# Kernel optimization log

Measured on AMD Instinct MI355X. Metric: run time of the kernel, lower is better.

Reference implementation:

```python
import jax, jax.numpy as jnp
import numpy as np
import math

B, S, H = 2, 2048, 2048
NQ, NKV, HD = 16, 4, 128
THETA = 10000.0


def rotate_half(x):
    x1, x2 = jnp.split(x, 2, axis=-1)
    return jnp.concatenate([-x2, x1], axis=-1)


def rope_cos_sin(position_ids, dim, base, dtype):
    # inv_freq: (dim/2,)
    inv_freq = 1.0 / (base ** (jnp.arange(0, dim, 2, dtype=jnp.float32) / dim))
    freqs = position_ids.astype(jnp.float32)[..., None] * inv_freq  # (B, S, dim/2)
    emb = jnp.concatenate([freqs, freqs], axis=-1)  # (B, S, dim)
    return jnp.cos(emb).astype(dtype), jnp.sin(emb).astype(dtype)


def setup_inputs() -> dict:
    key = jax.random.key(0)
    ks = jax.random.split(key, 5)
    hidden_states = jax.random.normal(ks[0], (B, S, H), dtype=jnp.float32)
    position_ids = jnp.broadcast_to(jnp.arange(S, dtype=jnp.int32)[None, :], (B, S))
    sc = 0.02
    wq = jax.random.normal(ks[1], (NQ * HD, H), dtype=jnp.float32) * sc
    wk = jax.random.normal(ks[2], (NKV * HD, H), dtype=jnp.float32) * sc
    wv = jax.random.normal(ks[3], (NKV * HD, H), dtype=jnp.float32) * sc
    wo = jax.random.normal(ks[4], (H, NQ * HD), dtype=jnp.float32) * sc
    return {"hidden_states": hidden_states, "position_ids": position_ids,
            "wq": wq, "wk": wk, "wv": wv, "wo": wo}


def reference(hidden_states, position_ids, wq, wk, wv, wo):
    b, s, _ = hidden_states.shape
    n_rep = NQ // NKV
    # QKV projections (no bias)
    q = (hidden_states @ wq.T).reshape(b, s, NQ, HD).transpose(0, 2, 1, 3)   # (b, nq, s, hd)
    k = (hidden_states @ wk.T).reshape(b, s, NKV, HD).transpose(0, 2, 1, 3)  # (b, nkv, s, hd)
    v = (hidden_states @ wv.T).reshape(b, s, NKV, HD).transpose(0, 2, 1, 3)
    # RoPE (full rotary, partial_rotary_factor == 1.0)
    cos, sin = rope_cos_sin(position_ids, HD, THETA, q.dtype)  # (b, s, hd)
    cos = cos[:, None, :, :]
    sin = sin[:, None, :, :]
    q = q * cos + rotate_half(q) * sin
    k = k * cos + rotate_half(k) * sin
    # repeat_kv for GQA: (b, nkv, s, hd) -> (b, nq, s, hd)
    k = jnp.repeat(k, n_rep, axis=1)
    v = jnp.repeat(v, n_rep, axis=1)
    # scores (b, nq, s, s)
    scores = jnp.einsum('bhqd,bhkd->bhqk', q, k) / math.sqrt(HD)
    causal = jnp.triu(jnp.full((s, s), -jnp.inf, dtype=scores.dtype), k=1)
    scores = scores + causal
    probs = jax.nn.softmax(scores.astype(jnp.float32), axis=-1).astype(q.dtype)
    out = jnp.einsum('bhqk,bhkd->bhqd', probs, v)  # (b, nq, s, hd)
    out = out.transpose(0, 2, 1, 3).reshape(b, s, NQ * HD)
    return out @ wo.T
```

## Files before the change

kernel.cpp:

```cpp
#include <hip/hip_runtime.h>
#include <hip/hip_bf16.h>
#include <cstdint>

typedef unsigned short u16;
typedef __attribute__((ext_vector_type(4))) float f32x4;
typedef __attribute__((ext_vector_type(8))) short s16x8;
typedef __attribute__((ext_vector_type(4))) unsigned int u32x4;
typedef __attribute__((ext_vector_type(2))) unsigned int u32x2;
typedef __attribute__((ext_vector_type(4))) unsigned short u16x4;
typedef __attribute__((ext_vector_type(8))) unsigned short u16x8;

#define MFMA16(a, b, c) __builtin_amdgcn_mfma_f32_16x16x32_bf16(a, b, c, 0, 0, 0)
#define GLOAD16(g, l) __builtin_amdgcn_global_load_lds((const __attribute__((address_space(1))) void*)(g), (__attribute__((address_space(3))) void*)(l), 16, 0, 0)

__device__ __forceinline__ u16 f2bf(float f) {
    union { float f; uint32_t u; } v{f};
    uint32_t r = v.u + 0x7FFF + ((v.u >> 16) & 1);
    return (u16)(r >> 16);
}
__device__ __forceinline__ float bf2f(u16 b) {
    union { uint32_t u; float f; } v;
    v.u = ((uint32_t)b) << 16;
    return v.f;
}

__global__ void cast_f32_bf16(const float* __restrict__ in, u16* __restrict__ out, int n4) {
    int i = blockIdx.x * 256 + threadIdx.x;
    if (i >= n4) return;
    float4 f = ((const float4*)in)[i];
    u16x4 o = { f2bf(f.x), f2bf(f.y), f2bf(f.z), f2bf(f.w) };
    ((u16x4*)out)[i] = o;
}

__global__ void rope_table_k(const int* __restrict__ pos, float* __restrict__ ct, float* __restrict__ st) {
    int i = blockIdx.x * 256 + threadIdx.x;
    int j = i & 63;
    int bs = i >> 6;
    float p = (float)pos[bs];
    float invf = powf(10000.0f, -(float)j * (1.0f / 64.0f));
    float ang = p * invf;
    ct[i] = cosf(ang);
    st[i] = sinf(ang);
}

template <int FUSE>
__global__ __launch_bounds__(256) void gemm_bt(const u16* __restrict__ A, const u16* __restrict__ Bw,
                                               float* __restrict__ C, int M, int N, int K,
                                               const float* __restrict__ ct, const float* __restrict__ st,
                                               u16* __restrict__ Qb, u16* __restrict__ Kb,
                                               u16* __restrict__ Vb) {
    __shared__ u16 Sh[128 * 128];
    u16* As = Sh;
    u16* Bs = Sh + 8192;
    const int tid = threadIdx.x;
    const int lane = tid & 63, wid = tid >> 6;
    const int g = lane >> 4, r = lane & 15;

    const int gx = gridDim.x, nwg = gx * gridDim.y;
    int lid = blockIdx.y * gx + blockIdx.x;
    int swz = (lid % 8) * (nwg / 8) + lid / 8;
    const int bxi = swz % gx, byi = swz / gx;

    const size_t bm = (size_t)byi * 128, bn = (size_t)bxi * 128;
    const int wr = (wid >> 1) * 64, wc = (wid & 1) * 64;

    const int srow = wid * 32 + (lane >> 3);
    const int schunk = (lane & 7) ^ ((lane >> 3) & 7);
    const u16* aSrc = A + (bm + srow) * (size_t)K + schunk * 8;
    const u16* bSrc = Bw + (bn + srow) * (size_t)K + schunk * 8;
    u16* aDst = As + wid * 2048;
    u16* bDst = Bs + wid * 2048;

    f32x4 acc[4][4] = {};
    for (int kt = 0; kt < K; kt += 64) {
#pragma unroll
        for (int j = 0; j < 4; ++j) {
            GLOAD16(aSrc + (size_t)(j * 8) * K + kt, aDst + j * 512);
            GLOAD16(bSrc + (size_t)(j * 8) * K + kt, bDst + j * 512);
        }
        __syncthreads();
        s16x8 af[4][2], bfr[4][2];
#pragma unroll
        for (int m = 0; m < 4; ++m)
#pragma unroll
            for (int kk = 0; kk < 2; ++kk) {
                int rowa = wr + m * 16 + r;
                af[m][kk] = *(const s16x8*)(As + rowa * 64 + (((kk * 4 + g) ^ (rowa & 7)) << 3));
                int rowb = wc + m * 16 + r;
                bfr[m][kk] = *(const s16x8*)(Bs + rowb * 64 + (((kk * 4 + g) ^ (rowb & 7)) << 3));
            }
#pragma unroll
        for (int m = 0; m < 4; ++m)
#pragma unroll
            for (int n = 0; n < 4; ++n) {
                acc[m][n] = MFMA16(af[m][0], bfr[n][0], acc[m][n]);
                acc[m][n] = MFMA16(af[m][1], bfr[n][1], acc[m][n]);
            }
        __syncthreads();
    }
    if (FUSE == 0) {
#pragma unroll
        for (int m = 0; m < 4; ++m)
#pragma unroll
            for (int n = 0; n < 4; ++n)
#pragma unroll
                for (int i = 0; i < 4; ++i) {
                    size_t row = bm + wr + m * 16 + g * 4 + i;
                    size_t col = bn + wc + n * 16 + r;
                    C[row * N + col] = acc[m][n][i];
                }
        return;
    }
#pragma unroll
    for (int m = 0; m < 4; ++m)
#pragma unroll
        for (int n = 0; n < 4; ++n)
#pragma unroll
            for (int i = 0; i < 4; ++i) {
                int rowl = wr + m * 16 + g * 4 + i;
                int col = wc + n * 16 + r;
                int c4 = col >> 3;
                *(u16*)((char*)Sh + rowl * 256 + (((c4 ^ (rowl & 15))) << 4) + ((col & 7) << 1)) =
                    f2bf(acc[m][n][i]);
            }
    __syncthreads();
    if (tid < 128) {
        const int hb = bxi;
        if (hb < 20) {
            const int rowl = tid;
            const size_t tok = bm + rowl;
            const int b = (int)(tok >> 11), s = (int)(tok & 2047);
            u16* dst;
            if (hb < 16) dst = Qb + (((size_t)(b * 16 + hb) * 2048 + s) << 7);
            else         dst = Kb + (((size_t)(b * 4 + (hb - 16)) * 2048 + s) << 7);
            const char* tb = (const char*)Sh + rowl * 256;
            const float* ctr = ct + tok * 64;
            const float* str = st + tok * 64;
#pragma unroll
            for (int c4 = 0; c4 < 8; ++c4) {
                u32x4 lo4 = *(const u32x4*)(tb + ((c4 ^ (rowl & 15)) << 4));
                u32x4 hi4 = *(const u32x4*)(tb + (((c4 + 8) ^ (rowl & 15)) << 4));
                const u16* lo = (const u16*)&lo4;
                const u16* hi = (const u16*)&hi4;
                u16x4 o0, o1, o2, o3;
                u16* olo[2] = { (u16*)&o0, (u16*)&o1 };
                u16* ohi[2] = { (u16*)&o2, (u16*)&o3 };
#pragma unroll
                for (int j = 0; j < 8; ++j) {
                    float c = ctr[c4 * 8 + j], sn = str[c4 * 8 + j];
                    float xl = bf2f(lo[j]), xh = bf2f(hi[j]);
                    olo[j >> 2][j & 3] = f2bf(xl * c - xh * sn);
                    ohi[j >> 2][j & 3] = f2bf(xh * c + xl * sn);
                }
                *(u16x4*)(dst + c4 * 8) = o0;
                *(u16x4*)(dst + c4 * 8 + 4) = o1;
                *(u16x4*)(dst + 64 + c4 * 8) = o2;
                *(u16x4*)(dst + 64 + c4 * 8 + 4) = o3;
            }
        } else {
            const int d = tid;
            const size_t tok0 = bm;
            const int b = (int)(tok0 >> 11), s0 = (int)(tok0 & 2047);
            u16* dst = Vb + (size_t)(b * 4 + (hb - 20)) * 262144 + (size_t)d * 2048 + s0;
            const int dslot = d >> 3, dbyte = (d & 7) << 1;
#pragma unroll
            for (int jb = 0; jb < 16; ++jb) {
                u16x8 v;
#pragma unroll
                for (int jj = 0; jj < 8; ++jj) {
                    int s = jb * 8 + jj;
                    v[jj] = *(const u16*)((const char*)Sh + s * 256 +
                                          (((dslot ^ (s & 15))) << 4) + dbyte);
                }
                *(u16x8*)(dst + jb * 8) = v;
            }
        }
    }
}

__global__ __launch_bounds__(256, 2) void attn_k(const u16* __restrict__ Qb, const u16* __restrict__ Kb,
                                                 const u16* __restrict__ Vb, u16* __restrict__ Ob) {
    __shared__ char smem[49152];
    u16* Ksh = (u16*)smem;
    u16* Vts = (u16*)(smem + 16384);
    char* Pall = smem + 32768;
    const int tid = threadIdx.x;
    const int lane = tid & 63, w = tid >> 6;
    const int g = lane >> 4, r = lane & 15;

    const int lid = blockIdx.y * gridDim.x + blockIdx.x;
    const int cpy = lid >> 8, p = lid & 255;
    const int bh = p & 31;
    const int qblk = cpy ? (7 - (p >> 5)) : ((p >> 5) + 8);

    const int b = bh >> 4, h = bh & 15;
    const int hkv = h >> 2;
    const int q0 = qblk * 128;
    const u16* Qh = Qb + ((size_t)(b * 16 + h) << 18);
    const u16* Kh = Kb + ((size_t)(b * 4 + hkv) << 18);
    const u16* Vh = Vb + ((size_t)(b * 4 + hkv) << 18);

    s16x8 qf[2][4];
#pragma unroll
    for (int qq = 0; qq < 2; ++qq)
#pragma unroll
        for (int c = 0; c < 4; ++c)
            qf[qq][c] = *(const s16x8*)(Qh + (size_t)(q0 + qq * 64 + w * 16 + r) * 128 + c * 32 + g * 8);

    f32x4 o[2][8] = {};
    float mrun[2] = {-1e30f, -1e30f};
    float lrun[2] = {0.f, 0.f};
    const int fmax[2] = { q0 + w * 16 + 15, q0 + 64 + w * 16 + 15 };

    const int ntiles = 2 * qblk + 2;
    const int krow0 = tid >> 4, kch = tid & 15;

    u32x4 kpr[4], vpr[4];
#pragma unroll
    for (int it = 0; it < 4; ++it)
        kpr[it] = *(const u32x4*)(Kh + (size_t)(krow0 + it * 16) * 128 + kch * 8);
#pragma unroll
    for (int it = 0; it < 4; ++it) {
        int task = tid + it * 256;
        vpr[it] = *(const u32x4*)(Vh + (size_t)(task >> 3) * 2048 + (task & 7) * 8);
    }

    for (int t = 0; t < ntiles; ++t) {
        const int kv0 = t * 64;
        __syncthreads();
#pragma unroll
        for (int it = 0; it < 4; ++it) {
            int row = krow0 + it * 16;
            *(u32x4*)((char*)Ksh + row * 256 + ((kch ^ (row & 7)) << 4)) = kpr[it];
        }
#pragma unroll
        for (int it = 0; it < 4; ++it) {
            int task = tid + it * 256;
            int d = task >> 3, ch = task & 7;
            *(u32x4*)((char*)Vts + d * 128 + ((ch ^ (d & 7) ^ ((d >> 3) & 7)) << 4)) = vpr[it];
        }
        __syncthreads();
        if (t + 1 < ntiles) {
            const int kn = kv0 + 64;
#pragma unroll
            for (int it = 0; it < 4; ++it)
                kpr[it] = *(const u32x4*)(Kh + (size_t)(kn + krow0 + it * 16) * 128 + kch * 8);
#pragma unroll
            for (int it = 0; it < 4; ++it) {
                int task = tid + it * 256;
                vpr[it] = *(const u32x4*)(Vh + (size_t)(task >> 3) * 2048 + kn + (task & 7) * 8);
            }
        }
        f32x4 st4[2][4];
#pragma unroll
        for (int ts = 0; ts < 4; ++ts) {
            int row = ts * 16 + r;
            s16x8 kf[4];
#pragma unroll
            for (int c = 0; c < 4; ++c)
                kf[c] = *(const s16x8*)((const char*)Ksh + row * 256 + (((c * 4 + g) ^ (row & 7)) << 4));
            f32x4 a0 = {}, a1 = {};
            if (kv0 <= fmax[0])
#pragma unroll
                for (int c = 0; c < 4; ++c) a0 = MFMA16(kf[c], qf[0][c], a0);
            if (kv0 <= fmax[1])
#pragma unroll
                for (int c = 0; c < 4; ++c) a1 = MFMA16(kf[c], qf[1][c], a1);
            st4[0][ts] = a0;
            st4[1][ts] = a1;
        }
#pragma unroll
        for (int qq = 0; qq < 2; ++qq) {
            if (kv0 > fmax[qq]) continue;
            const int qg = q0 + qq * 64 + w * 16 + r;
            float sv[16];
            float mtile = -1e30f;
#pragma unroll
            for (int ts = 0; ts < 4; ++ts)
#pragma unroll
                for (int i = 0; i < 4; ++i) {
                    int kvg = kv0 + ts * 16 + g * 4 + i;
                    float s = st4[qq][ts][i] * 0.08838834764831845f;
                    s = (kvg > qg) ? -1e30f : s;
                    sv[ts * 4 + i] = s;
                    mtile = fmaxf(mtile, s);
                }
            mtile = fmaxf(mtile, __shfl_xor(mtile, 16));
            mtile = fmaxf(mtile, __shfl_xor(mtile, 32));
            float mnew = fmaxf(mrun[qq], mtile);
            float corr = __expf(mrun[qq] - mnew);
            float psum = 0.f;
            unsigned int pw[8];
#pragma unroll
            for (int ts = 0; ts < 4; ++ts) {
                float p0 = __expf(sv[ts * 4 + 0] - mnew);
                float p1 = __expf(sv[ts * 4 + 1] - mnew);
                float p2 = __expf(sv[ts * 4 + 2] - mnew);
                float p3 = __expf(sv[ts * 4 + 3] - mnew);
                psum += (p0 + p1) + (p2 + p3);
                pw[ts * 2 + 0] = (unsigned int)f2bf(p0) | ((unsigned int)f2bf(p1) << 16);
                pw[ts * 2 + 1] = (unsigned int)f2bf(p2) | ((unsigned int)f2bf(p3) << 16);
            }
            psum += __shfl_xor(psum, 16);
            psum += __shfl_xor(psum, 32);
            lrun[qq] = lrun[qq] * corr + psum;
            mrun[qq] = mnew;
#pragma unroll
            for (int dsb = 0; dsb < 8; ++dsb)
#pragma unroll
                for (int i = 0; i < 4; ++i) o[qq][dsb][i] *= corr;
            char* pbase = Pall + (w * 2 + qq) * 2048;
#pragma unroll
            for (int ts = 0; ts < 4; ++ts) {
                int chunk = (ts * 2 + (g >> 1)) ^ (r & 7);
                u32x2 val = { pw[ts * 2], pw[ts * 2 + 1] };
                *(u32x2*)(pbase + r * 128 + chunk * 16 + (g & 1) * 8) = val;
            }
        }
        asm volatile("s_waitcnt lgkmcnt(0)" ::: "memory");
#pragma unroll
        for (int c = 0; c < 2; ++c) {
            s16x8 vf[8];
#pragma unroll
            for (int dsb = 0; dsb < 8; ++dsb) {
                int d = dsb * 16 + r;
                vf[dsb] = *(const s16x8*)((const char*)Vts + d * 128 +
                    ((((c * 4 + g) ^ (d & 7) ^ ((d >> 3) & 7))) << 4));
            }
#pragma unroll
            for (int qq = 0; qq < 2; ++qq) {
                if (kv0 > fmax[qq]) continue;
                s16x8 pf = *(const s16x8*)(Pall + (w * 2 + qq) * 2048 + r * 128 +
                                           (((c * 4 + g) ^ (r & 7)) << 4));
#pragma unroll
                for (int dsb = 0; dsb < 8; ++dsb)
                    o[qq][dsb] = MFMA16(vf[dsb], pf, o[qq][dsb]);
            }
        }
    }
    __syncthreads();
#pragma unroll
    for (int qq = 0; qq < 2; ++qq) {
        float linv = 1.0f / lrun[qq];
        char* obase = smem + (w << 13) + (qq << 12);
#pragma unroll
        for (int dsb = 0; dsb < 8; ++dsb)
#pragma unroll
            for (int i = 0; i < 4; ++i) {
                int d = dsb * 16 + g * 4 + i;
                *(u16*)(obase + r * 256 + d * 2) = f2bf(o[qq][dsb][i] * linv);
            }
    }
    asm volatile("s_waitcnt lgkmcnt(0)" ::: "memory");
    const int rr = lane >> 2, cbo = (lane & 3) * 32;
#pragma unroll
    for (int qq = 0; qq < 2; ++qq) {
        char* obase = smem + (w << 13) + (qq << 12);
        size_t oidx = ((size_t)b * 2048 + q0 + qq * 64 + w * 16 + rr) * 2048 + h * 128 + cbo;
#pragma unroll
        for (int p2 = 0; p2 < 4; ++p2) {
            u32x4 vv = *(const u32x4*)(obase + rr * 256 + cbo * 2 + p2 * 16);
            *(u32x4*)(Ob + oidx + p2 * 8) = vv;
        }
    }
}

extern "C" void kernel_launch(void* const* d_in, const int* in_sizes, int n_in,
                              void* d_out, int out_size, void* d_ws, size_t ws_size,
                              hipStream_t stream) {
    const float* hidden = (const float*)d_in[0];
    const int* pos = (const int*)d_in[1];
    const float* wq = (const float*)d_in[2];
    const float* wk = (const float*)d_in[3];
    const float* wv = (const float*)d_in[4];
    const float* wo = (const float*)d_in[5];
    float* out = (float*)d_out;

    char* ws = (char*)d_ws;
    size_t off = 0;
    auto alloc = [&](size_t bytes) { char* p = ws + off; off += (bytes + 255) & ~255ULL; return p; };
    u16* Xb   = (u16*)alloc(8388608ULL * 2);
    u16* WB   = (u16*)alloc(6291456ULL * 2);
    u16* WoB  = (u16*)alloc(4194304ULL * 2);
    u16* Qb   = (u16*)alloc(8388608ULL * 2);
    u16* Kb   = (u16*)alloc(2097152ULL * 2);
    u16* Vb   = (u16*)alloc(2097152ULL * 2);
    u16* Ab   = (u16*)alloc(8388608ULL * 2);
    float* ctab = (float*)alloc(262144ULL * 4);
    float* stab = (float*)alloc(262144ULL * 4);

    cast_f32_bf16<<<8192, 256, 0, stream>>>(hidden, Xb, 2097152);
    cast_f32_bf16<<<4096, 256, 0, stream>>>(wq, WB, 1048576);
    cast_f32_bf16<<<1024, 256, 0, stream>>>(wk, WB + 4194304, 262144);
    cast_f32_bf16<<<1024, 256, 0, stream>>>(wv, WB + 5242880, 262144);
    cast_f32_bf16<<<4096, 256, 0, stream>>>(wo, WoB, 1048576);
    rope_table_k<<<1024, 256, 0, stream>>>(pos, ctab, stab);
    gemm_bt<1><<<dim3(24, 32), 256, 0, stream>>>(Xb, WB, nullptr, 4096, 3072, 2048,
                                                 ctab, stab, Qb, Kb, Vb);
    attn_k<<<dim3(16, 32), 256, 0, stream>>>(Qb, Kb, Vb, Ab);
    gemm_bt<0><<<dim3(16, 32), 256, 0, stream>>>(Ab, WoB, out, 4096, 2048, 2048,
                                                 nullptr, nullptr, nullptr, nullptr, nullptr);
}
```

Before: 259.9 us.

## Double-buffer GEMM LDS tiles and transpose V epilogue in shared memory

The QKV/output GEMM now uses two LDS buffers, so the global-to-LDS loads for the next K tile are issued before the MFMA work on the current tile. The aim is to hide load latency behind compute. The V epilogue now writes accumulators transposed into LDS and then emits 16-byte vectorized global stores across all 256 threads, replacing the per-element gather done by 128 threads. Shared memory per block doubles to 64KB, which may lower occupancy.

```diff
diff --git a/kernel.cpp b/kernel.cpp
--- a/kernel.cpp
+++ b/kernel.cpp
@@ -49,9 +49,7 @@
                                                const float* __restrict__ ct, const float* __restrict__ st,
                                                u16* __restrict__ Qb, u16* __restrict__ Kb,
                                                u16* __restrict__ Vb) {
-    __shared__ u16 Sh[128 * 128];
-    u16* As = Sh;
-    u16* Bs = Sh + 8192;
+    __shared__ u16 Sh[32768];
     const int tid = threadIdx.x;
     const int lane = tid & 63, wid = tid >> 6;
     const int g = lane >> 4, r = lane & 15;
@@ -68,17 +66,25 @@
     const int schunk = (lane & 7) ^ ((lane >> 3) & 7);
     const u16* aSrc = A + (bm + srow) * (size_t)K + schunk * 8;
     const u16* bSrc = Bw + (bn + srow) * (size_t)K + schunk * 8;
-    u16* aDst = As + wid * 2048;
-    u16* bDst = Bs + wid * 2048;
+
+    auto STAGE = [&](int ktEl, int bi) {
+        u16* aD = Sh + bi * 16384 + wid * 2048;
+        u16* bD = Sh + bi * 16384 + 8192 + wid * 2048;
+#pragma unroll
+        for (int j = 0; j < 4; ++j) {
+            GLOAD16(aSrc + (size_t)(j * 8) * K + ktEl, aD + j * 512);
+            GLOAD16(bSrc + (size_t)(j * 8) * K + ktEl, bD + j * 512);
+        }
+    };
 
     f32x4 acc[4][4] = {};
-    for (int kt = 0; kt < K; kt += 64) {
-#pragma unroll
-        for (int j = 0; j < 4; ++j) {
-            GLOAD16(aSrc + (size_t)(j * 8) * K + kt, aDst + j * 512);
-            GLOAD16(bSrc + (size_t)(j * 8) * K + kt, bDst + j * 512);
-        }
-        __syncthreads();
+    const int nk = K >> 6;
+    STAGE(0, 0);
+    __syncthreads();
+    for (int t = 0; t < nk; ++t) {
+        if (t + 1 < nk) STAGE((t + 1) << 6, (t + 1) & 1);
+        const u16* As = Sh + (t & 1) * 16384;
+        const u16* Bs = As + 8192;
         s16x8 af[4][2], bfr[4][2];
 #pragma unroll
         for (int m = 0; m < 4; ++m)
@@ -111,22 +117,22 @@
                 }
         return;
     }
-#pragma unroll
-    for (int m = 0; m < 4; ++m)
-#pragma unroll
-        for (int n = 0; n < 4; ++n)
-#pragma unroll
-            for (int i = 0; i < 4; ++i) {
-                int rowl = wr + m * 16 + g * 4 + i;
-                int col = wc + n * 16 + r;
-                int c4 = col >> 3;
-                *(u16*)((char*)Sh + rowl * 256 + (((c4 ^ (rowl & 15))) << 4) + ((col & 7) << 1)) =
-                    f2bf(acc[m][n][i]);
-            }
-    __syncthreads();
-    if (tid < 128) {
-        const int hb = bxi;
-        if (hb < 20) {
+    const int hb = bxi;
+    if (hb < 20) {
+#pragma unroll
+        for (int m = 0; m < 4; ++m)
+#pragma unroll
+            for (int n = 0; n < 4; ++n)
+#pragma unroll
+                for (int i = 0; i < 4; ++i) {
+                    int rowl = wr + m * 16 + g * 4 + i;
+                    int col = wc + n * 16 + r;
+                    int c4 = col >> 3;
+                    *(u16*)((char*)Sh + rowl * 256 + (((c4 ^ (rowl & 15))) << 4) + ((col & 7) << 1)) =
+                        f2bf(acc[m][n][i]);
+                }
+        __syncthreads();
+        if (tid < 128) {
             const int rowl = tid;
             const size_t tok = bm + rowl;
             const int b = (int)(tok >> 11), s = (int)(tok & 2047);
@@ -157,23 +163,30 @@
                 *(u16x4*)(dst + 64 + c4 * 8) = o2;
                 *(u16x4*)(dst + 64 + c4 * 8 + 4) = o3;
             }
-        } else {
-            const int d = tid;
-            const size_t tok0 = bm;
-            const int b = (int)(tok0 >> 11), s0 = (int)(tok0 & 2047);
-            u16* dst = Vb + (size_t)(b * 4 + (hb - 20)) * 262144 + (size_t)d * 2048 + s0;
-            const int dslot = d >> 3, dbyte = (d & 7) << 1;
-#pragma unroll
-            for (int jb = 0; jb < 16; ++jb) {
-                u16x8 v;
-#pragma unroll
-                for (int jj = 0; jj < 8; ++jj) {
-                    int s = jb * 8 + jj;
-                    v[jj] = *(const u16*)((const char*)Sh + s * 256 +
-                                          (((dslot ^ (s & 15))) << 4) + dbyte);
-                }
-                *(u16x8*)(dst + jb * 8) = v;
-            }
+        }
+    } else {
+#pragma unroll
+        for (int m = 0; m < 4; ++m) {
+            int tokb = wr + m * 16 + g * 4;
+            int chunk = tokb >> 3;
+            int sub = (g & 1) * 8;
+#pragma unroll
+            for (int n = 0; n < 4; ++n) {
+                int d = wc + n * 16 + r;
+                u16x4 v = { f2bf(acc[m][n][0]), f2bf(acc[m][n][1]),
+                            f2bf(acc[m][n][2]), f2bf(acc[m][n][3]) };
+                *(u16x4*)((char*)Sh + d * 256 + (((chunk ^ (d & 15))) << 4) + sub) = v;
+            }
+        }
+        __syncthreads();
+        const int b = (int)(bm >> 11), s0 = (int)(bm & 2047);
+        u16* dst = Vb + (size_t)(b * 4 + (hb - 20)) * 262144;
+        const int dd = tid >> 1, half = (tid & 1) * 8;
+#pragma unroll
+        for (int c8 = 0; c8 < 8; ++c8) {
+            int sc = half + c8;
+            u32x4 v4 = *(const u32x4*)((const char*)Sh + dd * 256 + (((sc ^ (dd & 15))) << 4));
+            *(u32x4*)(dst + (size_t)dd * 2048 + s0 + sc * 8) = v4;
         }
     }
 }
```

Result: faster. 241.6 us (-7.0%).
